# Performance work log

Hardware: AMD Instinct MI355X
Metric: run time of the kernel (lower is better)

Reference implementation:

```python
import jax, jax.numpy as jnp
import numpy as np

T = 2048          # tokens (flattened prefill)
H = 3584          # hidden_size
NH = 16           # num query heads
NKV = 8           # num kv heads
G = NH // NKV     # GQA group size
D = 256           # head_dim
SCALE = 256.0 ** -0.5   # query_pre_attn_scalar ** -0.5
WINDOW = 1024     # sliding_window_size
CAP = 50.0        # logit softcap
BASE = 10000.0    # rope theta
NEG = -1e30


def _rope(x, positions):
    # x: [T, n, D], neox-style rotary over full head_dim
    half = D // 2
    inv_freq = 1.0 / (BASE ** (jnp.arange(0, D, 2, dtype=jnp.float32) / D))  # [half]
    ang = positions.astype(jnp.float32)[:, None] * inv_freq  # [T, half]
    cos = jnp.cos(ang)[:, None, :]  # [T,1,half]
    sin = jnp.sin(ang)[:, None, :]
    x1, x2 = x[..., :half], x[..., half:]
    return jnp.concatenate([x1 * cos - x2 * sin, x2 * cos + x1 * sin], axis=-1)


def setup_inputs() -> dict:
    key = jax.random.key(0)
    ks = jax.random.split(key, 5)
    s = 0.02
    return {
        "hidden_states": jax.random.normal(ks[0], (T, H), dtype=jnp.float32),
        "Wq": jax.random.normal(ks[1], (H, NH * D), dtype=jnp.float32) * s,
        "Wk": jax.random.normal(ks[2], (H, NKV * D), dtype=jnp.float32) * s,
        "Wv": jax.random.normal(ks[3], (H, NKV * D), dtype=jnp.float32) * s,
        "Wo": jax.random.normal(ks[4], (NH * D, H), dtype=jnp.float32) * s,
        "positions": jnp.arange(T, dtype=jnp.int32),
    }


def reference(hidden_states, Wq, Wk, Wv, Wo, positions):
    q = (hidden_states @ Wq).reshape(T, NH, D)
    k = (hidden_states @ Wk).reshape(T, NKV, D)
    v = (hidden_states @ Wv).reshape(T, NKV, D)
    q = _rope(q, positions)
    k = _rope(k, positions)

    # GQA attention: group query heads over kv heads
    qg = (q * SCALE).reshape(T, NKV, G, D)
    scores = jnp.einsum('qhgd,khd->hgqk', qg, k)  # [NKV,G,T,T]
    scores = CAP * jnp.tanh(scores / CAP)         # logit softcap

    i = jnp.arange(T)[:, None]
    j = jnp.arange(T)[None, :]
    mask = (j <= i) & (i - j < WINDOW)            # causal + sliding window
    scores = jnp.where(mask, scores, NEG)

    p = jax.nn.softmax(scores, axis=-1)
    o = jnp.einsum('hgqk,khd->qhgd', p, v).reshape(T, NH * D)
    return o @ Wo
```

## Files before the change

### kernel.cpp

```cpp
#include <hip/hip_runtime.h>
#include <math.h>

typedef __attribute__((ext_vector_type(8))) __bf16 bf16x8;
typedef __attribute__((ext_vector_type(4))) __bf16 bf16x4;
typedef __attribute__((ext_vector_type(4))) float f32x4;

#define TSEQ 2048
#define HDIM 3584
#define NQH  16
#define NKVH 8
#define DH   256
#define WIN  1024
#define QKD  (NQH * DH)
#define KVD  (NKVH * DH)
#define QLD  8256
#define OLD  4160
#define WOLD 4160
#define VLD  2112

#define MFMA __builtin_amdgcn_mfma_f32_16x16x32_bf16

__device__ __forceinline__ void gload_lds16(const void* g, void* l) {
  __builtin_amdgcn_global_load_lds(
      (const __attribute__((address_space(1))) void*)g,
      (__attribute__((address_space(3))) void*)l, 16, 0, 0);
}


__global__ void cvt_bf16_kernel(const float* __restrict__ in,
                                __bf16* __restrict__ out, long n) {
  long i = ((long)blockIdx.x * blockDim.x + threadIdx.x) * 4;
  if (i >= n) return;
  float4 v = *reinterpret_cast<const float4*>(in + i);
  bf16x4 o4;
  o4.x = (__bf16)v.x; o4.y = (__bf16)v.y; o4.z = (__bf16)v.z; o4.w = (__bf16)v.w;
  *reinterpret_cast<bf16x4*>(out + i) = o4;
}

__global__ void transpose_all_kernel(const float* __restrict__ Wq,
                                     const float* __restrict__ Wk,
                                     const float* __restrict__ Wv,
                                     const float* __restrict__ Wo,
                                     __bf16* __restrict__ WqT,
                                     __bf16* __restrict__ WkT,
                                     __bf16* __restrict__ WvT,
                                     __bf16* __restrict__ WoT) {
  __shared__ float tile[64][65];
  int id = blockIdx.x;
  const float* src; __bf16* dst; int R, C, ldo;
  if (id < 3584)      { src = Wq; dst = WqT; R = HDIM; C = QKD; ldo = HDIM; }
  else if (id < 5376) { id -= 3584; src = Wk; dst = WkT; R = HDIM; C = KVD; ldo = HDIM; }
  else if (id < 7168) { id -= 5376; src = Wv; dst = WvT; R = HDIM; C = KVD; ldo = HDIM; }
  else                { id -= 7168; src = Wo; dst = WoT; R = QKD; C = HDIM; ldo = WOLD; }
  const int nbx = C >> 6;
  const int c0 = (id % nbx) * 64, r0 = (id / nbx) * 64;
  const int tid = threadIdx.x;
#pragma unroll
  for (int it = 0; it < 4; ++it) {
    int f = tid + it * 256;
    int row = f >> 4, c4 = (f & 15) * 4;
    float4 v = *reinterpret_cast<const float4*>(&src[(size_t)(r0 + row) * C + c0 + c4]);
    tile[row][c4] = v.x; tile[row][c4 + 1] = v.y;
    tile[row][c4 + 2] = v.z; tile[row][c4 + 3] = v.w;
  }
  __syncthreads();
#pragma unroll
  for (int it = 0; it < 2; ++it) {
    int s = tid + it * 256;
    int oc = s >> 3, rb = (s & 7) * 8;
    bf16x8 o8;
#pragma unroll
    for (int j = 0; j < 8; ++j) o8[j] = (__bf16)tile[rb + j][oc];
    *reinterpret_cast<bf16x8*>(&dst[(size_t)(c0 + oc) * ldo + r0 + rb]) = o8;
  }
}

__global__ void transpose_bf16_kernel(const __bf16* __restrict__ in,
                                      __bf16* __restrict__ out, int ldin, int ldout) {
  __shared__ __bf16 tile[32][33];
  const int tx = threadIdx.x, ty = threadIdx.y;
  const int c0 = blockIdx.x * 32, r0 = blockIdx.y * 32;
#pragma unroll
  for (int i = 0; i < 4; ++i)
    tile[ty + i * 8][tx] = in[(size_t)(r0 + ty + i * 8) * ldin + (c0 + tx)];
  __syncthreads();
#pragma unroll
  for (int i = 0; i < 4; ++i)
    out[(size_t)(c0 + ty + i * 8) * ldout + (r0 + tx)] = tile[tx][ty + i * 8];
}

__global__ void rope_table_kernel(const int* __restrict__ positions,
                                  float* __restrict__ ct,
                                  float* __restrict__ st) {
  int i = blockIdx.x * blockDim.x + threadIdx.x;
  if (i >= TSEQ * 128) return;
  int t = i >> 7, j = i & 127;
  float invf = (float)exp((double)(-2 * j) * (9.210340371976184 / 256.0));
  float ang = (float)positions[t] * invf;
  ct[i] = cosf(ang);
  st[i] = sinf(ang);
}

__global__ void rope_qk_kernel(__bf16* __restrict__ qkv,
                               const float* __restrict__ ct,
                               const float* __restrict__ st) {
  int i = blockIdx.x * blockDim.x + threadIdx.x;
  int jg = (i & 15) * 8;
  int th = i >> 4;
  int t = th / 24;
  int hh = th - t * 24;
  float scale = (hh < 16) ? 0.0625f : 1.0f;
  size_t base = (size_t)t * QLD + ((hh < 16) ? hh * DH : QKD + (hh - 16) * DH) + jg;
  bf16x8 x1 = *reinterpret_cast<const bf16x8*>(qkv + base);
  bf16x8 x2 = *reinterpret_cast<const bf16x8*>(qkv + base + 128);
  const float* cp = ct + (t << 7) + jg;
  const float* sp = st + (t << 7) + jg;
  bf16x8 o1, o2;
#pragma unroll
  for (int e = 0; e < 8; ++e) {
    float c = cp[e], s = sp[e];
    float a = (float)x1[e], b = (float)x2[e];
    o1[e] = (__bf16)((a * c - b * s) * scale);
    o2[e] = (__bf16)((b * c + a * s) * scale);
  }
  *reinterpret_cast<bf16x8*>(qkv + base) = o1;
  *reinterpret_cast<bf16x8*>(qkv + base + 128) = o2;
}


__device__ __forceinline__ void stage_half(const __bf16* __restrict__ gbase,
                                           int row0, int ldg, int k0,
                                           __bf16* lds_half, int tid) {
  const int lane = tid & 63;
  const int w = tid >> 6;
  const int lr = lane >> 3;
  const int swzcol = ((lane & 7) ^ lr) << 3;
  const __bf16* g = gbase + (size_t)(row0 + w * 8 + lr) * ldg + k0 + swzcol;
  __bf16* l = lds_half + w * 512;
  gload_lds16(g, l);
  gload_lds16(g + (size_t)64 * ldg, l + 4096);
}

#define BAR __builtin_amdgcn_s_barrier()

#define RD_A(DST, BASE, MO)                                         \
  _Pragma("unroll")                                                 \
  for (int m_ = 0; m_ < 4; ++m_) {                                  \
    const __bf16* p_ = (BASE) + (((MO) + m_) * 16 + l15) * 64;      \
    DST[m_][0] = *(const bf16x8*)(p_ + kxa);                        \
    DST[m_][1] = *(const bf16x8*)(p_ + kxb);                        \
  }

#define RD_B(DST, BASE, NO)                                         \
  _Pragma("unroll")                                                 \
  for (int n_ = 0; n_ < 2; ++n_) {                                  \
    const __bf16* p_ = (BASE) + (bro + ((NO) + n_) * 16 + l15) * 64;\
    DST[n_][0] = *(const bf16x8*)(p_ + kxa);                        \
    DST[n_][1] = *(const bf16x8*)(p_ + kxb);                        \
  }

#define MQUAD(AF, BF, MO, NO)                                          \
  __builtin_amdgcn_s_setprio(1);                                       \
  _Pragma("unroll")                                                    \
  for (int m_ = 0; m_ < 4; ++m_)                                       \
    _Pragma("unroll")                                                  \
    for (int n_ = 0; n_ < 2; ++n_) {                                   \
      acc[(MO) + m_][(NO) + n_] =                                      \
          MFMA(AF[m_][0], BF[n_][0], acc[(MO) + m_][(NO) + n_], 0, 0, 0); \
      acc[(MO) + m_][(NO) + n_] =                                      \
          MFMA(AF[m_][1], BF[n_][1], acc[(MO) + m_][(NO) + n_], 0, 0, 0); \
    }                                                                  \
  __builtin_amdgcn_s_setprio(0);

__global__ __launch_bounds__(512, 2) void gemm256_kernel(
    const __bf16* __restrict__ A, const __bf16* __restrict__ B,
    __bf16* __restrict__ C, int lda, int Klen, int ldc, int nrc) {
  __shared__ __bf16 lds[2][2][2][8192];

  const int nwg = gridDim.x;
  const int per = nwg >> 3;
  const int wg = (blockIdx.x & 7) * per + (blockIdx.x >> 3);
  const int rem = wg % nrc;
  const int row0 = (rem & 7) * 256;
  const int col0 = (rem >> 3) * 256;
  __bf16* Cs = C;

  const int tid = threadIdx.x;
  const int lane = tid & 63, w = tid >> 6;
  const int wr = w >> 2, wc = w & 3;
  const int l15 = lane & 15, lg = lane >> 4;
  const int kxa = (lg * 8) ^ ((lane & 7) << 3);
  const int kxb = (32 + lg * 8) ^ ((lane & 7) << 3);
  const int bro = (wc & 1) * 64;

  const __bf16* Ablk = A + (size_t)row0 * lda;
  const __bf16* Bblk = B + (size_t)col0 * lda;

  const __bf16* Ae = &lds[0][0][wr][0];
  const __bf16* Be = &lds[0][1][wc >> 1][0];
  const __bf16* Ao = &lds[1][0][wr][0];
  const __bf16* Bo = &lds[1][1][wc >> 1][0];

  f32x4 acc[8][4] = {};
  const int NT = Klen >> 6;
  const int NI = NT >> 1;

  stage_half(Ablk, 0,   lda, 0,  &lds[0][0][0][0], tid);
  stage_half(Ablk, 128, lda, 0,  &lds[0][0][1][0], tid);
  stage_half(Bblk, 0,   lda, 0,  &lds[0][1][0][0], tid);
  stage_half(Bblk, 128, lda, 0,  &lds[0][1][1][0], tid);
  stage_half(Ablk, 0,   lda, 64, &lds[1][0][0][0], tid);
  stage_half(Ablk, 128, lda, 64, &lds[1][0][1][0], tid);
  asm volatile("s_waitcnt vmcnt(4)" ::: "memory");
  BAR;

  bf16x8 a03[4][2], a47[4][2], b01[2][2], b23[2][2];

  for (int j = 0; j < NI; ++j) {
    const int e = 2 * j, o = 2 * j + 1;
    const bool last = (j == NI - 1);

    RD_A(a03, Ae, 0);
    RD_B(b01, Be, 0);
    stage_half(Bblk, 0, lda, o * 64, &lds[1][1][0][0], tid);
    asm volatile("s_waitcnt lgkmcnt(8)" ::: "memory");
    BAR; MQUAD(a03, b01, 0, 0); BAR;

    RD_A(a47, Ae, 4);
    stage_half(Bblk, 128, lda, o * 64, &lds[1][1][1][0], tid);
    BAR; MQUAD(a47, b01, 4, 0); BAR;

    RD_B(b23, Be, 2);
    if (!last) stage_half(Ablk, 0, lda, (e + 2) * 64, &lds[0][0][0][0], tid);
    BAR; MQUAD(a47, b23, 4, 2); BAR;

    if (!last) {
      stage_half(Ablk, 128, lda, (e + 2) * 64, &lds[0][0][1][0], tid);
      asm volatile("s_waitcnt vmcnt(4)" ::: "memory");
    } else {
      asm volatile("s_waitcnt vmcnt(0)" ::: "memory");
    }
    BAR; MQUAD(a03, b23, 0, 2); BAR;

    RD_A(a03, Ao, 0);
    RD_B(b01, Bo, 0);
    if (!last) stage_half(Bblk, 0, lda, (e + 2) * 64, &lds[0][1][0][0], tid);
    asm volatile("s_waitcnt lgkmcnt(8)" ::: "memory");
    BAR; MQUAD(a03, b01, 0, 0); BAR;

    RD_A(a47, Ao, 4);
    if (!last) stage_half(Bblk, 128, lda, (e + 2) * 64, &lds[0][1][1][0], tid);
    BAR; MQUAD(a47, b01, 4, 0); BAR;

    RD_B(b23, Bo, 2);
    if (!last) stage_half(Ablk, 0, lda, (o + 2) * 64, &lds[1][0][0][0], tid);
    BAR; MQUAD(a47, b23, 4, 2); BAR;

    if (!last) {
      stage_half(Ablk, 128, lda, (o + 2) * 64, &lds[1][0][1][0], tid);
      asm volatile("s_waitcnt vmcnt(4)" ::: "memory");
    }
    BAR; MQUAD(a03, b23, 0, 2); BAR;
  }

#pragma unroll
  for (int m = 0; m < 8; ++m)
#pragma unroll
    for (int n = 0; n < 4; ++n)
#pragma unroll
      for (int r = 0; r < 4; ++r) {
        int row = row0 + wr * 128 + m * 16 + lg * 4 + r;
        int col = col0 + wc * 64 + n * 16 + l15;
        Cs[(size_t)row * ldc + col] = (__bf16)acc[m][n][r];
      }
}

__global__ __launch_bounds__(512, 1) void gemm128_kernel(
    const __bf16* __restrict__ A, const __bf16* __restrict__ B,
    float* __restrict__ C, int lda, int Klen, int ldc) {
  __shared__ __bf16 lds[2][3][8192];

  const int per = gridDim.x >> 3;
  const int wg = (blockIdx.x & 7) * per + (blockIdx.x >> 3);
  const int row0 = (wg & 15) * 128;
  const int col0 = (wg >> 4) * 256;

  const int tid = threadIdx.x;
  const int lane = tid & 63, w = tid >> 6;
  const int wr = w >> 2, wc = w & 3;
  const int l15 = lane & 15, lg = lane >> 4;
  const int kxa = (lg * 8) ^ ((lane & 7) << 3);
  const int kxb = (32 + lg * 8) ^ ((lane & 7) << 3);
  const int bro = (wc & 1) * 64;

  const __bf16* Ablk = A + (size_t)row0 * lda;
  const __bf16* Bblk = B + (size_t)col0 * lda;

  f32x4 acc[4][4] = {};
  const int NT = Klen >> 6;

  stage_half(Ablk, 0,   lda, 0,  &lds[0][0][0], tid);
  stage_half(Bblk, 0,   lda, 0,  &lds[0][1][0], tid);
  stage_half(Bblk, 128, lda, 0,  &lds[0][2][0], tid);
  stage_half(Ablk, 0,   lda, 64, &lds[1][0][0], tid);
  asm volatile("s_waitcnt vmcnt(2)" ::: "memory");
  BAR;

  bf16x8 a03[4][2], b01[2][2], b23[2][2];

  for (int t = 0; t < NT; ++t) {
    const int cur = t & 1, nxt = cur ^ 1;
    const __bf16* Ah = &lds[cur][0][0];
    const __bf16* Bh = &lds[cur][1 + (wc >> 1)][0];

    {
      const int MO = wr * 4;
#pragma unroll
      for (int m_ = 0; m_ < 4; ++m_) {
        const __bf16* p_ = Ah + ((MO + m_) * 16 + l15) * 64;
        a03[m_][0] = *(const bf16x8*)(p_ + kxa);
        a03[m_][1] = *(const bf16x8*)(p_ + kxb);
      }
    }
    RD_B(b01, Bh, 0);
    RD_B(b23, Bh, 2);

    if (t + 1 < NT) {
      stage_half(Bblk, 0,   lda, (t + 1) * 64, &lds[nxt][1][0], tid);
      stage_half(Bblk, 128, lda, (t + 1) * 64, &lds[nxt][2][0], tid);
    }

    asm volatile("s_waitcnt lgkmcnt(0)" ::: "memory");
    BAR;
    if (t + 2 < NT) stage_half(Ablk, 0, lda, (t + 2) * 64, &lds[cur][0][0], tid);

    __builtin_amdgcn_s_setprio(1);
#pragma unroll
    for (int m_ = 0; m_ < 4; ++m_) {
#pragma unroll
      for (int n_ = 0; n_ < 2; ++n_) {
        acc[m_][n_] = MFMA(a03[m_][0], b01[n_][0], acc[m_][n_], 0, 0, 0);
        acc[m_][n_] = MFMA(a03[m_][1], b01[n_][1], acc[m_][n_], 0, 0, 0);
        acc[m_][n_ + 2] = MFMA(a03[m_][0], b23[n_][0], acc[m_][n_ + 2], 0, 0, 0);
        acc[m_][n_ + 2] = MFMA(a03[m_][1], b23[n_][1], acc[m_][n_ + 2], 0, 0, 0);
      }
    }
    __builtin_amdgcn_s_setprio(0);

    if (t + 2 < NT) {
      asm volatile("s_waitcnt vmcnt(2)" ::: "memory");
    } else {
      asm volatile("s_waitcnt vmcnt(0)" ::: "memory");
    }
    BAR;
  }

#pragma unroll
  for (int m = 0; m < 4; ++m)
#pragma unroll
    for (int n = 0; n < 4; ++n)
#pragma unroll
      for (int r = 0; r < 4; ++r) {
        int row = row0 + wr * 64 + m * 16 + lg * 4 + r;
        int col = col0 + wc * 64 + n * 16 + l15;
        C[(size_t)row * ldc + col] = acc[m][n][r];
      }
}


__device__ __forceinline__ void attn_stage(const __bf16* __restrict__ kg,
                                           const __bf16* __restrict__ vg,
                                           __bf16* Kd, __bf16* Vd, int tid) {
#pragma unroll
  for (int i = 0; i < 8; ++i) {
    int c = tid + i * 256;
    int krow = c >> 5, kslot = c & 31;
    gload_lds16(kg + (size_t)krow * QLD + ((kslot ^ (krow & 7)) * 8), Kd + c * 8);
    int vrow = c >> 3, vslot = c & 7;
    gload_lds16(vg + (size_t)vrow * VLD + ((vslot ^ (vrow & 7)) * 8), Vd + c * 8);
  }
}

__global__ __launch_bounds__(256, 2) void attn_kernel(
    const __bf16* __restrict__ q, const __bf16* __restrict__ k,
    const __bf16* __restrict__ vt, __bf16* __restrict__ o) {
  __shared__ __bf16 Klds[64][256];
  __shared__ __bf16 Vlds[256][64];
  __shared__ __bf16 Plds[4][16][72];

  const int tid = threadIdx.x;
  const int wave = tid >> 6;
  const int lane = tid & 63;
  const int l16 = lane & 15;
  const int lg = lane >> 4;
  const int h = blockIdx.x;
  const int qh = 2 * h + (blockIdx.y & 1);
  const int q0 = (31 - (int)(blockIdx.y >> 1)) << 6;
  const int qr = q0 + wave * 16;

  const __bf16* kg0 = k + (size_t)h * DH;
  const __bf16* vg0 = vt + (size_t)(h * DH) * VLD;

  int t_lo = q0 - (WIN - 1);
  if (t_lo < 0) t_lo = 0;
  t_lo &= ~63;
  const int NTile = ((q0 - t_lo) >> 6) + 1;

  bf16x8 qf[8];
  {
    const __bf16* qp = q + (size_t)(qr + l16) * QLD + qh * DH + lg * 8;
#pragma unroll
    for (int ds = 0; ds < 8; ++ds)
      qf[ds] = *reinterpret_cast<const bf16x8*>(qp + ds * 32);
  }

  f32x4 accO[16] = {};
  float l_run[4] = {0.f, 0.f, 0.f, 0.f};

  for (int it = 0; it < NTile; ++it) {
    const int t0 = t_lo + it * 64;

    attn_stage(kg0 + (size_t)t0 * QLD, vg0 + t0, &Klds[0][0], &Vlds[0][0], tid);
    asm volatile("s_waitcnt vmcnt(0)" ::: "memory");
    __builtin_amdgcn_s_barrier();

    f32x4 accS[4] = {};
    __builtin_amdgcn_s_setprio(1);
#pragma unroll
    for (int ds = 0; ds < 8; ++ds)
#pragma unroll
      for (int nt = 0; nt < 4; ++nt) {
        int row = nt * 16 + l16;
        int slot = (4 * ds + lg) ^ (l16 & 7);
        bf16x8 kf = *reinterpret_cast<const bf16x8*>(&Klds[0][0] + row * 256 + slot * 8);
        accS[nt] = MFMA(qf[ds], kf, accS[nt], 0, 0, 0);
      }
    __builtin_amdgcn_s_setprio(0);

    float rs[4] = {0.f, 0.f, 0.f, 0.f};
#pragma unroll
    for (int nt = 0; nt < 4; ++nt) {
      int key = t0 + nt * 16 + l16;
#pragma unroll
      for (int r = 0; r < 4; ++r) {
        int row = qr + lg * 4 + r;
        float t = __expf(accS[nt][r] * 0.04f);
        float p = __expf(-100.0f / (t + 1.0f));
        bool valid = (key <= row) && (row - key < WIN);
        p = valid ? p : 0.f;
        rs[r] += p;
        Plds[wave][lg * 4 + r][nt * 16 + l16] = (__bf16)p;
      }
    }
#pragma unroll
    for (int off = 1; off < 16; off <<= 1)
#pragma unroll
      for (int r = 0; r < 4; ++r)
        rs[r] += __shfl_xor(rs[r], off);
#pragma unroll
    for (int r = 0; r < 4; ++r)
      l_run[r] += rs[r];

    __builtin_amdgcn_s_setprio(1);
#pragma unroll
    for (int ks = 0; ks < 2; ++ks) {
      bf16x8 pa = *reinterpret_cast<const bf16x8*>(&Plds[wave][l16][ks * 32 + lg * 8]);
#pragma unroll
      for (int nt2 = 0; nt2 < 16; ++nt2) {
        int row = nt2 * 16 + l16;
        int slot = (4 * ks + lg) ^ (l16 & 7);
        bf16x8 vb = *reinterpret_cast<const bf16x8*>(&Vlds[0][0] + row * 64 + slot * 8);
        accO[nt2] = MFMA(pa, vb, accO[nt2], 0, 0, 0);
      }
    }
    __builtin_amdgcn_s_setprio(0);
    __builtin_amdgcn_s_barrier();
  }

#pragma unroll
  for (int r = 0; r < 4; ++r) {
    float inv_l = 1.f / l_run[r];
    int row = qr + lg * 4 + r;
#pragma unroll
    for (int nt2 = 0; nt2 < 16; ++nt2)
      o[(size_t)row * OLD + qh * DH + nt2 * 16 + l16] = (__bf16)(accO[nt2][r] * inv_l);
  }
}


extern "C" void kernel_launch(void* const* d_in, const int* in_sizes, int n_in,
                              void* d_out, int out_size, void* d_ws, size_t ws_size,
                              hipStream_t stream) {
  const float* hs = (const float*)d_in[0];
  const float* Wq = (const float*)d_in[1];
  const float* Wk = (const float*)d_in[2];
  const float* Wv = (const float*)d_in[3];
  const float* Wo = (const float*)d_in[4];
  const int* positions = (const int*)d_in[5];
  float* out = (float*)d_out;

  char* ws = (char*)d_ws;
  const size_t SZ_HS  = (size_t)TSEQ * HDIM * 2;
  const size_t SZ_WQT = (size_t)QKD * HDIM * 2;
  const size_t SZ_WKT = (size_t)KVD * HDIM * 2;
  const size_t SZ_WOT = (size_t)HDIM * WOLD * 2;
  const size_t SZ_QKV = (size_t)TSEQ * QLD * 2;
  const size_t SZ_O   = (size_t)TSEQ * OLD * 2;
  const size_t SZ_VT  = (size_t)KVD * VLD * 2;
  const size_t SZ_TBL = (size_t)TSEQ * 128 * 4;

  __bf16* hs_bf = (__bf16*)ws; ws += SZ_HS;
  __bf16* WqT   = (__bf16*)ws; ws += SZ_WQT;
  __bf16* WkT   = (__bf16*)ws; ws += SZ_WKT;
  __bf16* WvT   = (__bf16*)ws; ws += SZ_WKT;
  __bf16* WoT   = (__bf16*)ws; ws += SZ_WOT;
  __bf16* qkv   = (__bf16*)ws; ws += SZ_QKV;
  __bf16* o_bf  = (__bf16*)ws; ws += SZ_O;
  __bf16* vt_bf = (__bf16*)ws; ws += SZ_VT;
  float*  cost  = (float*)ws;  ws += SZ_TBL;
  float*  sint  = (float*)ws;  ws += SZ_TBL;
  if ((size_t)(ws - (char*)d_ws) > ws_size) return;

  cvt_bf16_kernel<<<(TSEQ * HDIM) / 1024, 256, 0, stream>>>(hs, hs_bf, (long)TSEQ * HDIM);
  transpose_all_kernel<<<10752, 256, 0, stream>>>(Wq, Wk, Wv, Wo, WqT, WkT, WvT, WoT);
  rope_table_kernel<<<(TSEQ * 128) / 256, 256, 0, stream>>>(positions, cost, sint);

  gemm256_kernel<<<256, 512, 0, stream>>>(hs_bf, WqT, qkv, HDIM, HDIM, QLD, 256);

  rope_qk_kernel<<<(TSEQ * 24 * 16) / 256, 256, 0, stream>>>(qkv, cost, sint);
  transpose_bf16_kernel<<<dim3(KVD / 32, TSEQ / 32), dim3(32, 8), 0, stream>>>(qkv + QKD + KVD, vt_bf, QLD, VLD);

  attn_kernel<<<dim3(NKVH, 64), 256, 0, stream>>>(qkv, qkv + QKD, vt_bf, o_bf);

  gemm128_kernel<<<224, 512, 0, stream>>>(o_bf, WoT, out, OLD, QKD, HDIM);
}
```

Measured before the change: 304.5 us.

## Fuse RoPE and V transpose into QKV GEMM epilogue; merge prep kernels

The QKV projection GEMM epilogue now stages its output tile through LDS. For Q/K head columns it applies rotary embedding and the query scale before writing bf16. For V columns it writes the transposed layout straight into the vt buffer. This removes the separate rope and transpose kernels and their extra passes over qkv memory. The hidden-state fp32 to bf16 conversion is folded into the weight-transpose kernel to save a launch. LDS grows to about 132 KB, so launch bounds drop to one workgroup per CU, which may lower GEMM occupancy.

New measurement: 287.2 us. -5.7%, faster.

```diff
diff --git a/kernel.cpp b/kernel.cpp
--- a/kernel.cpp
+++ b/kernel.cpp
@@ -26,35 +26,36 @@
       (__attribute__((address_space(3))) void*)l, 16, 0, 0);
 }
 
-
-__global__ void cvt_bf16_kernel(const float* __restrict__ in,
-                                __bf16* __restrict__ out, long n) {
-  long i = ((long)blockIdx.x * blockDim.x + threadIdx.x) * 4;
-  if (i >= n) return;
-  float4 v = *reinterpret_cast<const float4*>(in + i);
-  bf16x4 o4;
-  o4.x = (__bf16)v.x; o4.y = (__bf16)v.y; o4.z = (__bf16)v.z; o4.w = (__bf16)v.w;
-  *reinterpret_cast<bf16x4*>(out + i) = o4;
-}
-
-__global__ void transpose_all_kernel(const float* __restrict__ Wq,
-                                     const float* __restrict__ Wk,
-                                     const float* __restrict__ Wv,
-                                     const float* __restrict__ Wo,
-                                     __bf16* __restrict__ WqT,
-                                     __bf16* __restrict__ WkT,
-                                     __bf16* __restrict__ WvT,
-                                     __bf16* __restrict__ WoT) {
+__global__ void prep_kernel(const float* __restrict__ hs,
+                            const float* __restrict__ Wq,
+                            const float* __restrict__ Wk,
+                            const float* __restrict__ Wv,
+                            const float* __restrict__ Wo,
+                            __bf16* __restrict__ hs_bf,
+                            __bf16* __restrict__ WqT,
+                            __bf16* __restrict__ WkT,
+                            __bf16* __restrict__ WvT,
+                            __bf16* __restrict__ WoT) {
   __shared__ float tile[64][65];
   int id = blockIdx.x;
-  const float* src; __bf16* dst; int R, C, ldo;
-  if (id < 3584)      { src = Wq; dst = WqT; R = HDIM; C = QKD; ldo = HDIM; }
-  else if (id < 5376) { id -= 3584; src = Wk; dst = WkT; R = HDIM; C = KVD; ldo = HDIM; }
-  else if (id < 7168) { id -= 5376; src = Wv; dst = WvT; R = HDIM; C = KVD; ldo = HDIM; }
-  else                { id -= 7168; src = Wo; dst = WoT; R = QKD; C = HDIM; ldo = WOLD; }
+  const int tid = threadIdx.x;
+  if (id >= 10752) {
+    long base = (long)(id - 10752) * 2048 + tid * 8;
+    float4 v0 = *reinterpret_cast<const float4*>(hs + base);
+    float4 v1 = *reinterpret_cast<const float4*>(hs + base + 4);
+    bf16x8 o8;
+    o8[0] = (__bf16)v0.x; o8[1] = (__bf16)v0.y; o8[2] = (__bf16)v0.z; o8[3] = (__bf16)v0.w;
+    o8[4] = (__bf16)v1.x; o8[5] = (__bf16)v1.y; o8[6] = (__bf16)v1.z; o8[7] = (__bf16)v1.w;
+    *reinterpret_cast<bf16x8*>(hs_bf + base) = o8;
+    return;
+  }
+  const float* src; __bf16* dst; int C, ldo;
+  if (id < 3584)      { src = Wq; dst = WqT; C = QKD; ldo = HDIM; }
+  else if (id < 5376) { id -= 3584; src = Wk; dst = WkT; C = KVD; ldo = HDIM; }
+  else if (id < 7168) { id -= 5376; src = Wv; dst = WvT; C = KVD; ldo = HDIM; }
+  else                { id -= 7168; src = Wo; dst = WoT; C = HDIM; ldo = WOLD; }
   const int nbx = C >> 6;
   const int c0 = (id % nbx) * 64, r0 = (id / nbx) * 64;
-  const int tid = threadIdx.x;
 #pragma unroll
   for (int it = 0; it < 4; ++it) {
     int f = tid + it * 256;
@@ -73,20 +74,6 @@
     for (int j = 0; j < 8; ++j) o8[j] = (__bf16)tile[rb + j][oc];
     *reinterpret_cast<bf16x8*>(&dst[(size_t)(c0 + oc) * ldo + r0 + rb]) = o8;
   }
-}
-
-__global__ void transpose_bf16_kernel(const __bf16* __restrict__ in,
-                                      __bf16* __restrict__ out, int ldin, int ldout) {
-  __shared__ __bf16 tile[32][33];
-  const int tx = threadIdx.x, ty = threadIdx.y;
-  const int c0 = blockIdx.x * 32, r0 = blockIdx.y * 32;
-#pragma unroll
-  for (int i = 0; i < 4; ++i)
-    tile[ty + i * 8][tx] = in[(size_t)(r0 + ty + i * 8) * ldin + (c0 + tx)];
-  __syncthreads();
-#pragma unroll
-  for (int i = 0; i < 4; ++i)
-    out[(size_t)(c0 + ty + i * 8) * ldout + (r0 + tx)] = tile[tx][ty + i * 8];
 }
 
 __global__ void rope_table_kernel(const int* __restrict__ positions,
@@ -99,32 +86,6 @@
   float ang = (float)positions[t] * invf;
   ct[i] = cosf(ang);
   st[i] = sinf(ang);
-}
-
-__global__ void rope_qk_kernel(__bf16* __restrict__ qkv,
-                               const float* __restrict__ ct,
-                               const float* __restrict__ st) {
-  int i = blockIdx.x * blockDim.x + threadIdx.x;
-  int jg = (i & 15) * 8;
-  int th = i >> 4;
-  int t = th / 24;
-  int hh = th - t * 24;
-  float scale = (hh < 16) ? 0.0625f : 1.0f;
-  size_t base = (size_t)t * QLD + ((hh < 16) ? hh * DH : QKD + (hh - 16) * DH) + jg;
-  bf16x8 x1 = *reinterpret_cast<const bf16x8*>(qkv + base);
-  bf16x8 x2 = *reinterpret_cast<const bf16x8*>(qkv + base + 128);
-  const float* cp = ct + (t << 7) + jg;
-  const float* sp = st + (t << 7) + jg;
-  bf16x8 o1, o2;
-#pragma unroll
-  for (int e = 0; e < 8; ++e) {
-    float c = cp[e], s = sp[e];
-    float a = (float)x1[e], b = (float)x2[e];
-    o1[e] = (__bf16)((a * c - b * s) * scale);
-    o2[e] = (__bf16)((b * c + a * s) * scale);
-  }
-  *reinterpret_cast<bf16x8*>(qkv + base) = o1;
-  *reinterpret_cast<bf16x8*>(qkv + base + 128) = o2;
 }
 
 
@@ -172,10 +133,14 @@
     }                                                                  \
   __builtin_amdgcn_s_setprio(0);
 
-__global__ __launch_bounds__(512, 2) void gemm256_kernel(
+#define STG(p, ab, h) (lds + (p) * 32768 + (ab) * 16384 + (h) * 8192)
+
+__global__ __launch_bounds__(512, 1) void gemm256_kernel(
     const __bf16* __restrict__ A, const __bf16* __restrict__ B,
-    __bf16* __restrict__ C, int lda, int Klen, int ldc, int nrc) {
-  __shared__ __bf16 lds[2][2][2][8192];
+    __bf16* __restrict__ C, __bf16* __restrict__ vt,
+    const float* __restrict__ ct, const float* __restrict__ st,
+    int lda, int Klen, int ldc, int nrc) {
+  __shared__ __bf16 lds[67584];
 
   const int nwg = gridDim.x;
   const int per = nwg >> 3;
@@ -183,7 +148,6 @@
   const int rem = wg % nrc;
   const int row0 = (rem & 7) * 256;
   const int col0 = (rem >> 3) * 256;
-  __bf16* Cs = C;
 
   const int tid = threadIdx.x;
   const int lane = tid & 63, w = tid >> 6;
@@ -196,21 +160,21 @@
   const __bf16* Ablk = A + (size_t)row0 * lda;
   const __bf16* Bblk = B + (size_t)col0 * lda;
 
-  const __bf16* Ae = &lds[0][0][wr][0];
-  const __bf16* Be = &lds[0][1][wc >> 1][0];
-  const __bf16* Ao = &lds[1][0][wr][0];
-  const __bf16* Bo = &lds[1][1][wc >> 1][0];
+  const __bf16* Ae = STG(0, 0, wr);
+  const __bf16* Be = STG(0, 1, wc >> 1);
+  const __bf16* Ao = STG(1, 0, wr);
+  const __bf16* Bo = STG(1, 1, wc >> 1);
 
   f32x4 acc[8][4] = {};
   const int NT = Klen >> 6;
   const int NI = NT >> 1;
 
-  stage_half(Ablk, 0,   lda, 0,  &lds[0][0][0][0], tid);
-  stage_half(Ablk, 128, lda, 0,  &lds[0][0][1][0], tid);
-  stage_half(Bblk, 0,   lda, 0,  &lds[0][1][0][0], tid);
-  stage_half(Bblk, 128, lda, 0,  &lds[0][1][1][0], tid);
-  stage_half(Ablk, 0,   lda, 64, &lds[1][0][0][0], tid);
-  stage_half(Ablk, 128, lda, 64, &lds[1][0][1][0], tid);
+  stage_half(Ablk, 0,   lda, 0,  STG(0, 0, 0), tid);
+  stage_half(Ablk, 128, lda, 0,  STG(0, 0, 1), tid);
+  stage_half(Bblk, 0,   lda, 0,  STG(0, 1, 0), tid);
+  stage_half(Bblk, 128, lda, 0,  STG(0, 1, 1), tid);
+  stage_half(Ablk, 0,   lda, 64, STG(1, 0, 0), tid);
+  stage_half(Ablk, 128, lda, 64, STG(1, 0, 1), tid);
   asm volatile("s_waitcnt vmcnt(4)" ::: "memory");
   BAR;
 
@@ -222,20 +186,20 @@
 
     RD_A(a03, Ae, 0);
     RD_B(b01, Be, 0);
-    stage_half(Bblk, 0, lda, o * 64, &lds[1][1][0][0], tid);
+    stage_half(Bblk, 0, lda, o * 64, STG(1, 1, 0), tid);
     asm volatile("s_waitcnt lgkmcnt(8)" ::: "memory");
     BAR; MQUAD(a03, b01, 0, 0); BAR;
 
     RD_A(a47, Ae, 4);
-    stage_half(Bblk, 128, lda, o * 64, &lds[1][1][1][0], tid);
+    stage_half(Bblk, 128, lda, o * 64, STG(1, 1, 1), tid);
     BAR; MQUAD(a47, b01, 4, 0); BAR;
 
     RD_B(b23, Be, 2);
-    if (!last) stage_half(Ablk, 0, lda, (e + 2) * 64, &lds[0][0][0][0], tid);
+    if (!last) stage_half(Ablk, 0, lda, (e + 2) * 64, STG(0, 0, 0), tid);
     BAR; MQUAD(a47, b23, 4, 2); BAR;
 
     if (!last) {
-      stage_half(Ablk, 128, lda, (e + 2) * 64, &lds[0][0][1][0], tid);
+      stage_half(Ablk, 128, lda, (e + 2) * 64, STG(0, 0, 1), tid);
       asm volatile("s_waitcnt vmcnt(4)" ::: "memory");
     } else {
       asm volatile("s_waitcnt vmcnt(0)" ::: "memory");
@@ -244,35 +208,80 @@
 
     RD_A(a03, Ao, 0);
     RD_B(b01, Bo, 0);
-    if (!last) stage_half(Bblk, 0, lda, (e + 2) * 64, &lds[0][1][0][0], tid);
+    if (!last) stage_half(Bblk, 0, lda, (e + 2) * 64, STG(0, 1, 0), tid);
     asm volatile("s_waitcnt lgkmcnt(8)" ::: "memory");
     BAR; MQUAD(a03, b01, 0, 0); BAR;
 
     RD_A(a47, Ao, 4);
-    if (!last) stage_half(Bblk, 128, lda, (e + 2) * 64, &lds[0][1][1][0], tid);
+    if (!last) stage_half(Bblk, 128, lda, (e + 2) * 64, STG(0, 1, 1), tid);
     BAR; MQUAD(a47, b01, 4, 0); BAR;
 
     RD_B(b23, Bo, 2);
-    if (!last) stage_half(Ablk, 0, lda, (o + 2) * 64, &lds[1][0][0][0], tid);
+    if (!last) stage_half(Ablk, 0, lda, (o + 2) * 64, STG(1, 0, 0), tid);
     BAR; MQUAD(a47, b23, 4, 2); BAR;
 
     if (!last) {
-      stage_half(Ablk, 128, lda, (o + 2) * 64, &lds[1][0][1][0], tid);
+      stage_half(Ablk, 128, lda, (o + 2) * 64, STG(1, 0, 1), tid);
       asm volatile("s_waitcnt vmcnt(4)" ::: "memory");
     }
     BAR; MQUAD(a03, b23, 0, 2); BAR;
   }
 
-#pragma unroll
-  for (int m = 0; m < 8; ++m)
-#pragma unroll
-    for (int n = 0; n < 4; ++n)
-#pragma unroll
-      for (int r = 0; r < 4; ++r) {
-        int row = row0 + wr * 128 + m * 16 + lg * 4 + r;
-        int col = col0 + wc * 64 + n * 16 + l15;
-        Cs[(size_t)row * ldc + col] = (__bf16)acc[m][n][r];
-      }
+  const int head = col0 >> 8;
+  if (head < 24) {
+    const float scale = (head < 16) ? 0.0625f : 1.0f;
+#pragma unroll
+    for (int m = 0; m < 8; ++m)
+#pragma unroll
+      for (int n = 0; n < 4; ++n)
+#pragma unroll
+        for (int r = 0; r < 4; ++r) {
+          int rw = wr * 128 + m * 16 + lg * 4 + r;
+          int cl = wc * 64 + n * 16 + l15;
+          lds[rw * 256 + cl] = (__bf16)acc[m][n][r];
+        }
+    __syncthreads();
+#pragma unroll
+    for (int it8 = 0; it8 < 8; ++it8) {
+      int g = it8 * 512 + tid;
+      int rw = g >> 4, d0 = (g & 15) * 8;
+      bf16x8 x1 = *reinterpret_cast<const bf16x8*>(&lds[rw * 256 + d0]);
+      bf16x8 x2 = *reinterpret_cast<const bf16x8*>(&lds[rw * 256 + 128 + d0]);
+      int t = row0 + rw;
+      const float* cp = ct + t * 128 + d0;
+      const float* sp = st + t * 128 + d0;
+      bf16x8 o1, o2;
+#pragma unroll
+      for (int e2 = 0; e2 < 8; ++e2) {
+        float c = cp[e2], s = sp[e2];
+        float a = (float)x1[e2], b = (float)x2[e2];
+        o1[e2] = (__bf16)((a * c - b * s) * scale);
+        o2[e2] = (__bf16)((b * c + a * s) * scale);
+      }
+      *reinterpret_cast<bf16x8*>(&C[(size_t)t * ldc + col0 + d0]) = o1;
+      *reinterpret_cast<bf16x8*>(&C[(size_t)t * ldc + col0 + 128 + d0]) = o2;
+    }
+  } else {
+#pragma unroll
+    for (int m = 0; m < 8; ++m)
+#pragma unroll
+      for (int n = 0; n < 4; ++n)
+#pragma unroll
+        for (int r = 0; r < 4; ++r) {
+          int rw = wr * 128 + m * 16 + lg * 4 + r;
+          int cl = wc * 64 + n * 16 + l15;
+          lds[cl * 264 + rw] = (__bf16)acc[m][n][r];
+        }
+    __syncthreads();
+    const int vbase = (head - 24) * 256;
+#pragma unroll
+    for (int it16 = 0; it16 < 16; ++it16) {
+      int g = it16 * 512 + tid;
+      int d = g >> 5, rg = (g & 31) * 8;
+      bf16x8 v8 = *reinterpret_cast<const bf16x8*>(&lds[d * 264 + rg]);
+      *reinterpret_cast<bf16x8*>(&vt[(size_t)(vbase + d) * VLD + row0 + rg]) = v8;
+    }
+  }
 }
 
 __global__ __launch_bounds__(512, 1) void gemm128_kernel(
@@ -366,7 +375,6 @@
         C[(size_t)row * ldc + col] = acc[m][n][r];
       }
 }
-
 
 __device__ __forceinline__ void attn_stage(const __bf16* __restrict__ kg,
                                            const __bf16* __restrict__ vg,
@@ -521,14 +529,12 @@
   float*  sint  = (float*)ws;  ws += SZ_TBL;
   if ((size_t)(ws - (char*)d_ws) > ws_size) return;
 
-  cvt_bf16_kernel<<<(TSEQ * HDIM) / 1024, 256, 0, stream>>>(hs, hs_bf, (long)TSEQ * HDIM);
-  transpose_all_kernel<<<10752, 256, 0, stream>>>(Wq, Wk, Wv, Wo, WqT, WkT, WvT, WoT);
+  prep_kernel<<<14336, 256, 0, stream>>>(hs, Wq, Wk, Wv, Wo, hs_bf,
+                                         WqT, WkT, WvT, WoT);
   rope_table_kernel<<<(TSEQ * 128) / 256, 256, 0, stream>>>(positions, cost, sint);
 
-  gemm256_kernel<<<256, 512, 0, stream>>>(hs_bf, WqT, qkv, HDIM, HDIM, QLD, 256);
-
-  rope_qk_kernel<<<(TSEQ * 24 * 16) / 256, 256, 0, stream>>>(qkv, cost, sint);
-  transpose_bf16_kernel<<<dim3(KVD / 32, TSEQ / 32), dim3(32, 8), 0, stream>>>(qkv + QKD + KVD, vt_bf, QLD, VLD);
+  gemm256_kernel<<<256, 512, 0, stream>>>(hs_bf, WqT, qkv, vt_bf, cost, sint,
+                                          HDIM, HDIM, QLD, 256);
 
   attn_kernel<<<dim3(NKVH, 64), 256, 0, stream>>>(qkv, qkv + QKD, vt_bf, o_bf);
 
```
